# Optimization experiments

Measured on AMD Instinct MI355X. Metric: run time of the kernel, lower is better.

The kernel has to match this reference:

```python
import jax, jax.numpy as jnp
import numpy as np

C = 384          # input_channels
DH = 768         # dim_hidden
WS = 7           # window size (kernel_size)
NH = 12          # num_heads
HID = 3072       # mlp hidden = dim_hidden * mlp_ratio
NP = WS * WS     # 49 patch tokens
N = NP + 1       # + 1 cls token
SCALE = (C // NH) ** -0.5
REL_DIM = 2 * WS - 1


def _rel_pos_index():
    r = np.arange(WS)
    qx, qy = np.meshgrid(r, r, indexing='ij')
    q = np.stack([qx.ravel(), qy.ravel()], -1)                 # [NP,2], row-major flatten
    rel = q[:, None, :] - q[None, :, :] + WS - 1               # [NP,NP,2], values in [0,2ws-2]
    return jnp.asarray(rel[..., 0] * REL_DIM + rel[..., 1])    # [NP,NP]

REL_IDX = _rel_pos_index()


def layer_norm(x, g, b, eps=1e-5):
    m = jnp.mean(x, axis=-1, keepdims=True)
    v = jnp.var(x, axis=-1, keepdims=True)
    return (x - m) * jax.lax.rsqrt(v + eps) * g + b


def attention(x, w_qkv, w_proj, b_proj, rel_pos=None, mask=None):
    Bx, Nx, Cx = x.shape
    qkv = (x @ w_qkv.T).reshape(Bx, Nx, 3, NH, Cx // NH).transpose(2, 0, 3, 1, 4)
    q, k, v = qkv[0], qkv[1], qkv[2]                           # [B,H,N,d]
    attn = jnp.einsum('bhqd,bhkd->bhqk', q, k) * SCALE
    if rel_pos is not None:
        bias = rel_pos[REL_IDX].transpose(2, 0, 1)[None]       # [1,NH,NP,NP]
        attn = attn.at[:, :, 1:, 1:].add(bias)                 # skip cls token row/col
    if mask is not None:
        attn = attn + mask[:, None]                            # broadcast over heads
    attn = jax.nn.softmax(attn, axis=-1)
    y = jnp.einsum('bhqk,bhkd->bhqd', attn, v).transpose(0, 2, 1, 3).reshape(Bx, Nx, Cx)
    return y @ w_proj.T + b_proj


def setup_inputs() -> dict:
    key = jax.random.key(0)
    ks = jax.random.split(key, 16)
    s = 0.02
    BNW = 2048  # B * num_windows = 32 * 64
    return {
        'out': jax.random.normal(ks[0], (BNW, N, C), jnp.float32),
        'mask': jnp.zeros((BNW, N, N), jnp.float32),
        'g0': jnp.ones((C,), jnp.float32), 'b0': jnp.zeros((C,), jnp.float32),
        'g1': jnp.ones((C,), jnp.float32), 'b1': jnp.zeros((C,), jnp.float32),
        'g2': jnp.ones((C,), jnp.float32), 'b2': jnp.zeros((C,), jnp.float32),
        'ge': jnp.ones((C,), jnp.float32), 'be': jnp.zeros((C,), jnp.float32),
        'w_qkv': jax.random.normal(ks[1], (3 * C, C), jnp.float32) * s,
        'w_proj': jax.random.normal(ks[2], (C, C), jnp.float32) * s,
        'b_proj': jnp.zeros((C,), jnp.float32),
        'rel_pos': jax.random.normal(ks[3], (REL_DIM * REL_DIM, NH), jnp.float32) * s,
        'w_fc1': jax.random.normal(ks[4], (HID, C), jnp.float32) * s,
        'b_fc1': jnp.zeros((HID,), jnp.float32),
        'w_fc2': jax.random.normal(ks[5], (DH, HID), jnp.float32) * s,
        'b_fc2': jnp.zeros((DH,), jnp.float32),
        'w_exp': jax.random.normal(ks[6], (DH, C), jnp.float32) * s,
        'b_exp': jnp.zeros((DH,), jnp.float32),
        'w_lin': jax.random.normal(ks[7], (C, DH), jnp.float32) * s,
        'b_lin': jnp.zeros((C,), jnp.float32),
        'B': 32, 'H': 56, 'W': 56,
    }


def reference(out, mask, g0, b0, g1, b1, g2, b2, ge, be,
              w_qkv, w_proj, b_proj, rel_pos,
              w_fc1, b_fc1, w_fc2, b_fc2, w_exp, b_exp, w_lin, b_lin,
              B, H, W):
    Cc = out.shape[-1]
    # cls-token attention across windows of each image
    cls = out[:, :1].reshape(B, -1, Cc)                        # [B, nw, C]
    cls = cls + attention(layer_norm(cls, g0, b0), w_qkv, w_proj, b_proj)
    cls = cls.reshape(-1, 1, Cc)
    x = jnp.concatenate([cls, out[:, 1:]], axis=1)             # [B*nw, N, C]
    # windowed patch attention with rel-pos bias + mask
    x = x + attention(layer_norm(x, g1, b1), w_qkv, w_proj, b_proj,
                      rel_pos=rel_pos, mask=mask)
    # expand path: norm -> gelu -> linear (input_channels != dim_hidden)
    identity = jax.nn.gelu(layer_norm(x, ge, be), approximate=False) @ w_exp.T + b_exp
    # mlp path: norm -> fc1 -> gelu -> fc2
    h = layer_norm(x, g2, b2)
    h = jax.nn.gelu(h @ w_fc1.T + b_fc1, approximate=False)
    h = h @ w_fc2.T + b_fc2
    tmp = identity + h                                          # [B*nw, N, DH]
    return tmp @ w_lin.T + b_lin                                # [B*nw, N, C]
```

## Files before the change

kernel.cpp:

```cpp
#include <hip/hip_runtime.h>
#include <hip/hip_bf16.h>
#include <math.h>

#define NHEADS 12
#define NTOK   50
#define NWIN   2048
#define IMGS   32
#define CDIM   384
#define QKVD   1152
#define DHID   768
#define MLPH   3072
#define KTAIL  3456
#define SCALE_F 0.17677669529663687f

typedef short short8 __attribute__((ext_vector_type(8)));
typedef short short4v __attribute__((ext_vector_type(4)));
typedef short short2v __attribute__((ext_vector_type(2)));
typedef float f32x4  __attribute__((ext_vector_type(4)));
typedef __hip_bfloat16 bf16;

__device__ __forceinline__ float gelu_f(float x){
  return 0.5f*x*(1.0f+erff(x*0.7071067811865476f));
}
__device__ __forceinline__ short bfs(float x){
  bf16 h = __float2bfloat16(x); return *(short*)&h;
}

__global__ void cvt4_kernel(const float* s0, bf16* d0, int n0,
                            const float* s1, bf16* d1, int n1,
                            const float* s2, bf16* d2, int n2,
                            const float* s3, bf16* d3, int n3){
  int stride = gridDim.x*blockDim.x, g = blockIdx.x*blockDim.x + threadIdx.x;
  for (int i=g; i<n0; i+=stride) d0[i] = __float2bfloat16(s0[i]);
  for (int i=g; i<n1; i+=stride) d1[i] = __float2bfloat16(s1[i]);
  for (int i=g; i<n2; i+=stride) d2[i] = __float2bfloat16(s2[i]);
  for (int i=g; i<n3; i+=stride) d3[i] = __float2bfloat16(s3[i]);
}

__global__ __launch_bounds__(256) void transpose_cvt_kernel(const float* __restrict__ src,
    bf16* __restrict__ dst, int R, int Cc){
  __shared__ float tile[32][33];
  int bx = blockIdx.x, by = blockIdx.y;
  int c = threadIdx.x & 31, r0 = threadIdx.x >> 5;
  #pragma unroll
  for (int rr = r0; rr < 32; rr += 8)
    tile[rr][c] = src[(size_t)(by*32+rr)*Cc + bx*32 + c];
  __syncthreads();
  #pragma unroll
  for (int rr = r0; rr < 32; rr += 8)
    dst[(size_t)(bx*32+rr)*R + by*32 + c] = __float2bfloat16(tile[c][rr]);
}

__global__ void bias_combine_kernel(const float* __restrict__ wlin,
    const float* __restrict__ b_lin, const float* __restrict__ b_exp,
    const float* __restrict__ b_fc2, float* __restrict__ biasc){
  int i = blockIdx.x*blockDim.x + threadIdx.x;
  if (i >= CDIM) return;
  float s = b_lin[i];
  for (int d=0; d<DHID; d++) s += wlin[(size_t)i*DHID+d]*(b_exp[d]+b_fc2[d]);
  biasc[i] = s;
}

template<bool GELU>
__global__ __launch_bounds__(256) void ln_kernel(const float* __restrict__ x, long ldx,
    const float* __restrict__ g, const float* __restrict__ b,
    bf16* __restrict__ y, int rows)
{
  int row = blockIdx.x*4 + (threadIdx.x>>6);
  if (row >= rows) return;
  int l = threadIdx.x & 63;
  const float2* xr = (const float2*)(x + (size_t)row*ldx);
  float2 v[3]; float s = 0.f;
  #pragma unroll
  for (int j=0;j<3;j++){ v[j] = xr[l + 64*j]; s += v[j].x + v[j].y; }
  #pragma unroll
  for (int off=32; off; off>>=1) s += __shfl_xor(s, off, 64);
  float mean = s * (1.0f/384.0f);
  float vs = 0.f;
  #pragma unroll
  for (int j=0;j<3;j++){ float dx=v[j].x-mean, dy=v[j].y-mean; vs += dx*dx+dy*dy; }
  #pragma unroll
  for (int off=32; off; off>>=1) vs += __shfl_xor(vs, off, 64);
  float rstd = rsqrtf(vs*(1.0f/384.0f) + 1e-5f);
  short2v* yr = (short2v*)(y + (size_t)row*384);
  const float2* gv = (const float2*)g; const float2* bv = (const float2*)b;
  #pragma unroll
  for (int j=0;j<3;j++){
    float2 gg = gv[l+64*j], bb = bv[l+64*j];
    float o0 = (v[j].x-mean)*rstd*gg.x + bb.x;
    float o1 = (v[j].y-mean)*rstd*gg.y + bb.y;
    if (GELU){ o0 = gelu_f(o0); o1 = gelu_f(o1); }
    short2v pk; pk[0]=bfs(o0); pk[1]=bfs(o1);
    yr[l+64*j] = pk;
  }
}

__global__ __launch_bounds__(256) void ln_dual_kernel(const float* __restrict__ x,
    const float* __restrict__ ge, const float* __restrict__ be,
    const float* __restrict__ g2, const float* __restrict__ b2,
    bf16* __restrict__ yeo, long lde, bf16* __restrict__ y2o, int rows)
{
  int row = blockIdx.x*4 + (threadIdx.x>>6);
  if (row >= rows) return;
  int l = threadIdx.x & 63;
  const float2* xr = (const float2*)(x + (size_t)row*384);
  float2 v[3]; float s = 0.f;
  #pragma unroll
  for (int j=0;j<3;j++){ v[j] = xr[l + 64*j]; s += v[j].x + v[j].y; }
  #pragma unroll
  for (int off=32; off; off>>=1) s += __shfl_xor(s, off, 64);
  float mean = s * (1.0f/384.0f);
  float vs = 0.f;
  #pragma unroll
  for (int j=0;j<3;j++){ float dx=v[j].x-mean, dy=v[j].y-mean; vs += dx*dx+dy*dy; }
  #pragma unroll
  for (int off=32; off; off>>=1) vs += __shfl_xor(vs, off, 64);
  float rstd = rsqrtf(vs*(1.0f/384.0f) + 1e-5f);
  short2v* ye = (short2v*)(yeo + (size_t)row*lde);
  short2v* y2 = (short2v*)(y2o + (size_t)row*384);
  const float2* gev = (const float2*)ge; const float2* bev = (const float2*)be;
  const float2* g2v = (const float2*)g2; const float2* b2v = (const float2*)b2;
  #pragma unroll
  for (int j=0;j<3;j++){
    float n0 = (v[j].x-mean)*rstd, n1 = (v[j].y-mean)*rstd;
    float2 gg = gev[l+64*j], bb = bev[l+64*j];
    short2v pe; pe[0]=bfs(gelu_f(n0*gg.x+bb.x)); pe[1]=bfs(gelu_f(n1*gg.y+bb.y));
    ye[l+64*j] = pe;
    gg = g2v[l+64*j]; bb = b2v[l+64*j];
    short2v p2; p2[0]=bfs(n0*gg.x+bb.x); p2[1]=bfs(n1*gg.y+bb.y);
    y2[l+64*j] = p2;
  }
}

template<bool OUT_BF16, bool BIAS, int RES, bool GELU>
__device__ __forceinline__ void gemm_dev(
    const bf16* __restrict__ A, const bf16* __restrict__ B, void* Cv,
    const float* __restrict__ bias, const void* res,
    int M, int N, int K, int ldc, int ldres)
{
  __shared__ short As[3][128*32];
  __shared__ short Bs[3][128*32];
  const int t  = threadIdx.x;
  const int l  = t & 63;
  const int w  = t >> 6;
  const int wr = w >> 1, wc = w & 1;
  const int lr = l & 15, kg = l >> 4;

  const int nwg = gridDim.x * gridDim.y;
  const int lin = blockIdx.y * gridDim.x + blockIdx.x;
  const int q8 = nwg >> 3, r8 = nwg & 7;
  const int xcd = lin & 7, slot = lin >> 3;
  const int swz = (xcd < r8) ? (xcd*(q8+1) + slot) : (r8*(q8+1) + (xcd-r8)*q8 + slot);
  const int by = swz / gridDim.x, bx = swz - by*gridDim.x;

  const int bm = by * 128, bn = bx * 128;
  const short* Ag = (const short*)A;
  const short* Bg = (const short*)B;

  const int eo0 = w*1024 + l*8;
  const int rowS0 = eo0 >> 5, colS0 = eo0 & 31;
  const int eo1 = eo0 + 512;
  const int rowS1 = eo1 >> 5, colS1 = eo1 & 31;

  #define STAGE(k0, b) do { \
    __builtin_amdgcn_global_load_lds( \
      (const __attribute__((address_space(1))) void*)&Ag[(size_t)(bm+rowS0)*K + (k0) + colS0], \
      (__attribute__((address_space(3))) void*)((char*)&As[b][0] + w*2048), 16, 0, 0); \
    __builtin_amdgcn_global_load_lds( \
      (const __attribute__((address_space(1))) void*)&Bg[(size_t)(bn+rowS0)*K + (k0) + colS0], \
      (__attribute__((address_space(3))) void*)((char*)&Bs[b][0] + w*2048), 16, 0, 0); \
    __builtin_amdgcn_global_load_lds( \
      (const __attribute__((address_space(1))) void*)&Ag[(size_t)(bm+rowS1)*K + (k0) + colS1], \
      (__attribute__((address_space(3))) void*)((char*)&As[b][0] + w*2048 + 1024), 16, 0, 0); \
    __builtin_amdgcn_global_load_lds( \
      (const __attribute__((address_space(1))) void*)&Bg[(size_t)(bn+rowS1)*K + (k0) + colS1], \
      (__attribute__((address_space(3))) void*)((char*)&Bs[b][0] + w*2048 + 1024), 16, 0, 0); \
  } while(0)

  f32x4 acc[4][4] = {};

  STAGE(0, 0);
  STAGE(32, 1);
  asm volatile("s_waitcnt vmcnt(4)" ::: "memory");
  __builtin_amdgcn_s_barrier();

  int cur = 0, nb = 2;
  for (int k0 = 0; k0 < K; k0 += 32) {
    const bool more = (k0 + 64 < K);
    if (more) STAGE(k0 + 64, nb);

    short8 af[4], bfm[4];
    #pragma unroll
    for (int m=0;m<4;m++) af[m]  = *(const short8*)(&As[cur][(wr*64 + m*16 + lr)*32 + kg*8]);
    #pragma unroll
    for (int n=0;n<4;n++) bfm[n] = *(const short8*)(&Bs[cur][(wc*64 + n*16 + lr)*32 + kg*8]);
    __builtin_amdgcn_s_setprio(1);
    #pragma unroll
    for (int m=0;m<4;m++)
      #pragma unroll
      for (int n=0;n<4;n++)
        acc[m][n] = __builtin_amdgcn_mfma_f32_16x16x32_bf16(af[m], bfm[n], acc[m][n], 0,0,0);
    __builtin_amdgcn_s_setprio(0);

    if (more) { asm volatile("s_waitcnt vmcnt(4)" ::: "memory"); }
    else      { asm volatile("s_waitcnt vmcnt(0)" ::: "memory"); }
    __builtin_amdgcn_s_barrier();
    cur = (cur==2) ? 0 : cur+1;
    nb  = (nb==2)  ? 0 : nb+1;
  }
  #undef STAGE

  #pragma unroll
  for (int m=0;m<4;m++){
    int row0 = bm + wr*64 + m*16 + kg*4;
    #pragma unroll
    for (int n=0;n<4;n++){
      int col = bn + wc*64 + n*16 + lr;
      float bv = BIAS ? bias[col] : 0.0f;
      #pragma unroll
      for (int r=0;r<4;r++){
        float val = acc[m][n][r] + bv;
        if (RES == 1) val += ((const float*)res)[(size_t)(row0+r)*ldres + col];
        if (GELU) val = gelu_f(val);
        if (OUT_BF16) ((bf16*)Cv)[(size_t)(row0+r)*ldc + col] = __float2bfloat16(val);
        else          ((float*)Cv)[(size_t)(row0+r)*ldc + col] = val;
      }
    }
  }
}

#define GEMM_K(NAME, OB, BI, RE, GE) \
__global__ __launch_bounds__(256) void NAME( \
    const bf16* __restrict__ A, const bf16* __restrict__ B, void* Cv, \
    const float* __restrict__ bias, const void* res, \
    int M, int N, int K, int ldc, int ldres){ \
  gemm_dev<OB,BI,RE,GE>(A,B,Cv,bias,res,M,N,K,ldc,ldres); }

GEMM_K(gemm_qkv_k,  true,  false, 0, false)
GEMM_K(gemm_proj_k, false, true,  1, false)
GEMM_K(gemm_fc1_k,  true,  true,  0, true)
GEMM_K(gemm_tail_k, false, true,  0, false)
GEMM_K(gemm_wcmb_k, true,  false, 0, false)

__global__ __launch_bounds__(256) void attn_cls_kernel(const bf16* __restrict__ qkv,
                                                       bf16* __restrict__ y)
{
  int img = blockIdx.x, h = blockIdx.y;
  __shared__ float q[64][33], k[64][33], v[64][33];
  __shared__ float s[64][65];
  int t = threadIdx.x;
  for (int idx=t; idx<64*32; idx+=256){
    int i = idx>>5, d = idx&31;
    const bf16* base = qkv + ((size_t)(img*64+i))*QKVD + h*32 + d;
    q[i][d] = __bfloat162float(base[0]);
    k[i][d] = __bfloat162float(base[384]);
    v[i][d] = __bfloat162float(base[768]);
  }
  __syncthreads();
  for (int idx=t; idx<64*64; idx+=256){
    int i = idx>>6, j = idx&63;
    float a = 0.f;
    #pragma unroll
    for (int d=0; d<32; d++) a += q[i][d]*k[j][d];
    s[i][j] = a * SCALE_F;
  }
  __syncthreads();
  if (t < 64){
    float m = -1e30f;
    for (int j=0;j<64;j++) m = fmaxf(m, s[t][j]);
    float sum = 0.f;
    for (int j=0;j<64;j++){ float e = __expf(s[t][j]-m); s[t][j]=e; sum+=e; }
    float inv = 1.0f/sum;
    for (int j=0;j<64;j++) s[t][j] *= inv;
  }
  __syncthreads();
  for (int idx=t; idx<64*32; idx+=256){
    int i = idx>>5, d = idx&31;
    float a = 0.f;
    for (int j=0;j<64;j++) a += s[i][j]*v[j][d];
    y[((size_t)(img*64+i))*CDIM + h*32 + d] = __float2bfloat16(a);
  }
}

__global__ __launch_bounds__(64) void attn_win_mfma(const bf16* __restrict__ qkv,
    const float* __restrict__ mask, const float* __restrict__ rel_pos,
    bf16* __restrict__ y)
{
  const int lw = blockIdx.x, h = blockIdx.y;
  const int l = threadIdx.x;
  const int lr = l & 15, kg = l >> 4;
  __shared__ short Plds[64*72];
  __shared__ short VTl[32*72];
  __shared__ float rp[169];

  const size_t tok0 = (size_t)lw * NTOK;
  const short* qbase = (const short*)qkv;

  for (int i=l; i<169; i+=64) rp[i] = rel_pos[i*NHEADS + h];

  short8 qf[4], kf[4];
  #pragma unroll
  for (int n=0;n<4;n++){
    int qt = 16*n + lr;
    if (qt < 50) qf[n] = *(const short8*)&qbase[(tok0+qt)*QKVD + h*32 + kg*8];
    else         qf[n] = short8(0);
  }
  #pragma unroll
  for (int m=0;m<4;m++){
    int kt = 16*m + lr;
    if (kt < 50) kf[m] = *(const short8*)&qbase[(tok0+kt)*QKVD + 384 + h*32 + kg*8];
    else         kf[m] = short8(0);
  }

  {
    short vv[32];
    if (l < 50){
      const short8* vp = (const short8*)&qbase[(tok0+l)*QKVD + 768 + h*32];
      #pragma unroll
      for (int jj=0;jj<4;jj++){ short8 xv = vp[jj];
        #pragma unroll
        for (int e=0;e<8;e++) vv[jj*8+e] = xv[e]; }
    } else {
      #pragma unroll
      for (int d=0; d<32; d++) vv[d]=0;
    }
    #pragma unroll
    for (int d=0; d<32; d++) VTl[d*72 + l] = vv[d];
  }

  f32x4 sacc[4][4] = {};
  #pragma unroll
  for (int m=0;m<4;m++)
    #pragma unroll
    for (int n=0;n<4;n++)
      sacc[m][n] = __builtin_amdgcn_mfma_f32_16x16x32_bf16(kf[m], qf[n], sacc[m][n], 0,0,0);

  const float* mrow = mask + (size_t)lw*2500;
  float sv[4][4][4];
  #pragma unroll
  for (int m=0;m<4;m++){
    #pragma unroll
    for (int r=0;r<4;r++){
      int kt = 16*m + 4*kg + r;
      #pragma unroll
      for (int n=0;n<4;n++){
        int qt = 16*n + lr;
        float a;
        if (kt < 50 && qt < 50){
          a = sacc[m][n][r] * SCALE_F;
          if (kt>=1 && qt>=1){
            int qi=qt-1, kj=kt-1;
            int ridx = ((qi/7)-(kj/7)+6)*13 + (qi%7)-(kj%7)+6;
            a += rp[ridx];
          }
          a += mrow[qt*50+kt];
        } else a = -1e30f;
        sv[m][r][n] = a;
      }
    }
  }

  #pragma unroll
  for (int n=0;n<4;n++){
    float mx = -1e30f;
    #pragma unroll
    for (int m=0;m<4;m++)
      #pragma unroll
      for (int r=0;r<4;r++) mx = fmaxf(mx, sv[m][r][n]);
    mx = fmaxf(mx, __shfl_xor(mx, 16));
    mx = fmaxf(mx, __shfl_xor(mx, 32));
    float sum = 0.f;
    float pv[4][4];
    #pragma unroll
    for (int m=0;m<4;m++)
      #pragma unroll
      for (int r=0;r<4;r++){ float p = __expf(sv[m][r][n]-mx); pv[m][r]=p; sum+=p; }
    sum += __shfl_xor(sum, 16);
    sum += __shfl_xor(sum, 32);
    float inv = 1.0f/sum;
    int qrow = (16*n + lr)*72;
    #pragma unroll
    for (int m=0;m<4;m++){
      short4v pk;
      #pragma unroll
      for (int r=0;r<4;r++) pk[r] = bfs(pv[m][r]*inv);
      *(short4v*)&Plds[qrow + 16*m + 4*kg] = pk;
    }
  }
  __syncthreads();

  f32x4 oacc[2][4] = {};
  #pragma unroll
  for (int ks=0; ks<2; ks++){
    short8 pf[4];
    #pragma unroll
    for (int n=0;n<4;n++)
      pf[n] = *(const short8*)&Plds[(16*n+lr)*72 + 32*ks + kg*8];
    #pragma unroll
    for (int md=0; md<2; md++){
      short8 vf = *(const short8*)&VTl[(16*md+lr)*72 + 32*ks + kg*8];
      #pragma unroll
      for (int n=0;n<4;n++)
        oacc[md][n] = __builtin_amdgcn_mfma_f32_16x16x32_bf16(vf, pf[n], oacc[md][n], 0,0,0);
    }
  }

  short* yb = (short*)y;
  #pragma unroll
  for (int n=0;n<4;n++){
    int qt = 16*n + lr;
    if (qt >= 50) continue;
    #pragma unroll
    for (int md=0; md<2; md++){
      short4v pk;
      #pragma unroll
      for (int r=0;r<4;r++) pk[r] = bfs(oacc[md][n][r]);
      *(short4v*)&yb[(tok0+qt)*CDIM + h*32 + 16*md + 4*kg] = pk;
    }
  }
}

extern "C" void kernel_launch(void* const* d_in, const int* in_sizes, int n_in,
                              void* d_out, int out_size, void* d_ws, size_t ws_size,
                              hipStream_t stream)
{
  const float* x_in   = (const float*)d_in[0];
  const float* maskp  = (const float*)d_in[1];
  const float* g0 = (const float*)d_in[2];  const float* b0 = (const float*)d_in[3];
  const float* g1 = (const float*)d_in[4];  const float* b1 = (const float*)d_in[5];
  const float* g2 = (const float*)d_in[6];  const float* b2 = (const float*)d_in[7];
  const float* ge = (const float*)d_in[8];  const float* be = (const float*)d_in[9];
  const float* w_qkv = (const float*)d_in[10];
  const float* w_proj= (const float*)d_in[11];
  const float* b_proj= (const float*)d_in[12];
  const float* rel_pos=(const float*)d_in[13];
  const float* w_fc1 = (const float*)d_in[14];
  const float* b_fc1 = (const float*)d_in[15];
  const float* w_fc2 = (const float*)d_in[16];
  const float* b_fc2 = (const float*)d_in[17];
  const float* w_exp = (const float*)d_in[18];
  const float* b_exp = (const float*)d_in[19];
  const float* w_lin = (const float*)d_in[20];
  const float* b_lin = (const float*)d_in[21];
  float* dout = (float*)d_out;

  const size_t NT = (size_t)NWIN * NTOK;

  size_t off = 0;
  auto alloc = [&](size_t bytes)->void* {
    void* p = (char*)d_ws + off;
    off += (bytes + 255) & ~(size_t)255;
    return p;
  };

  bf16* wqkv_b = (bf16*)alloc((size_t)QKVD*CDIM*2);
  bf16* wproj_b= (bf16*)alloc((size_t)CDIM*CDIM*2);
  bf16* wfc1_b = (bf16*)alloc((size_t)MLPH*CDIM*2);
  bf16* wlin_b = (bf16*)alloc((size_t)CDIM*DHID*2);
  bf16* wexpT_b= (bf16*)alloc((size_t)CDIM*DHID*2);
  bf16* wfc2T_b= (bf16*)alloc((size_t)MLPH*DHID*2);
  bf16* W_comb = (bf16*)alloc((size_t)CDIM*KTAIL*2);
  float* biasc = (float*)alloc((size_t)CDIM*4);
  float* xb    = (float*)alloc(NT*CDIM*4);
  bf16* clsln  = (bf16*)alloc((size_t)NWIN*CDIM*2);
  bf16* qkvcls = (bf16*)alloc((size_t)NWIN*QKVD*2);
  bf16* ycls   = (bf16*)alloc((size_t)NWIN*CDIM*2);

  int CH_W = 2048;
  const size_t per_window = 537600ull;
  while (CH_W > 128 && off + (size_t)CH_W*per_window + 16384 > ws_size) CH_W >>= 1;
  const int CH_T = CH_W * NTOK;

  bf16*  xln   = (bf16*) alloc((size_t)CH_T*CDIM*2);
  bf16*  qkvc  = (bf16*) alloc((size_t)CH_T*QKVD*2);
  bf16*  ybfc  = (bf16*) alloc((size_t)CH_T*CDIM*2);
  bf16*  h1ext = (bf16*) alloc((size_t)CH_T*KTAIL*2);

  cvt4_kernel<<<512, 256, 0, stream>>>(
      w_qkv, wqkv_b, QKVD*CDIM,  w_proj, wproj_b, CDIM*CDIM,
      w_fc1, wfc1_b, MLPH*CDIM,  w_lin,  wlin_b,  CDIM*DHID);
  transpose_cvt_kernel<<<dim3(CDIM/32, DHID/32), 256, 0, stream>>>(w_exp, wexpT_b, DHID, CDIM);
  transpose_cvt_kernel<<<dim3(MLPH/32, DHID/32), 256, 0, stream>>>(w_fc2, wfc2T_b, DHID, MLPH);
  bias_combine_kernel<<<6, 64, 0, stream>>>(w_lin, b_lin, b_exp, b_fc2, biasc);
  gemm_wcmb_k<<<dim3(CDIM/128, CDIM/128), 256, 0, stream>>>(
      wlin_b, wexpT_b, W_comb, nullptr, nullptr, CDIM, CDIM, DHID, KTAIL, 0);
  gemm_wcmb_k<<<dim3(MLPH/128, CDIM/128), 256, 0, stream>>>(
      wlin_b, wfc2T_b, W_comb + 384, nullptr, nullptr, CDIM, MLPH, DHID, KTAIL, 0);

  hipMemcpyAsync(xb, x_in, NT*CDIM*4, hipMemcpyDeviceToDevice, stream);

  ln_kernel<false><<<NWIN/4, 256, 0, stream>>>(x_in, (long)NTOK*CDIM, g0, b0, clsln, NWIN);
  gemm_qkv_k<<<dim3(QKVD/128, NWIN/128), 256, 0, stream>>>(
      clsln, wqkv_b, qkvcls, nullptr, nullptr, NWIN, QKVD, CDIM, QKVD, 0);
  attn_cls_kernel<<<dim3(IMGS, NHEADS), 256, 0, stream>>>(qkvcls, ycls);
  gemm_proj_k<<<dim3(CDIM/128, NWIN/128), 256, 0, stream>>>(
      ycls, wproj_b, xb, b_proj, x_in, NWIN, CDIM, CDIM, NTOK*CDIM, NTOK*CDIM);

  const int nch = NWIN / CH_W;
  for (int c = 0; c < nch; c++){
    int w0 = c * CH_W;
    size_t t0 = (size_t)w0 * NTOK;
    float* xbc = xb + t0*CDIM;
    float* doutc = dout + t0*CDIM;
    int MT = CH_T, MB = CH_T/128;

    ln_kernel<false><<<MT/4, 256, 0, stream>>>(xbc, CDIM, g1, b1, xln, MT);
    gemm_qkv_k<<<dim3(QKVD/128, MB), 256, 0, stream>>>(
        xln, wqkv_b, qkvc, nullptr, nullptr, MT, QKVD, CDIM, QKVD, 0);
    attn_win_mfma<<<dim3(CH_W, NHEADS), 64, 0, stream>>>(
        qkvc, maskp + (size_t)w0*2500, rel_pos, ybfc);
    gemm_proj_k<<<dim3(CDIM/128, MB), 256, 0, stream>>>(
        ybfc, wproj_b, xbc, b_proj, xbc, MT, CDIM, CDIM, CDIM, CDIM);

    ln_dual_kernel<<<MT/4, 256, 0, stream>>>(xbc, ge, be, g2, b2, h1ext, KTAIL, ybfc, MT);

    gemm_fc1_k<<<dim3(MLPH/128, MB), 256, 0, stream>>>(
        ybfc, wfc1_b, h1ext + 384, b_fc1, nullptr, MT, MLPH, CDIM, KTAIL, 0);

    gemm_tail_k<<<dim3(CDIM/128, MB), 256, 0, stream>>>(
        h1ext, W_comb, doutc, biasc, nullptr, MT, CDIM, KTAIL, CDIM, 0);
  }
}
```

Baseline: 1.826 ms.

## Fuse fc1+GELU with folded fc2/lin GEMM, keeping hidden activations on-chip

Replaces the fc1 GEMM that wrote a 3072-wide bf16 hidden buffer, and the separate tail GEMM that re-read it, with one fused kernel. Each 64-row block computes fc1+GELU in 128-column chunks into LDS and accumulates immediately into the pre-folded W_lin·W_fc2 product. The expand path becomes a separate small GEMM that writes the output first, and the fused kernel adds onto it. This removes large HBM round trips for the hidden activations and shrinks workspace. In exchange it reads the weights from global memory per block without LDS staging, and uses 64-row blocks with heavy register use, which may limit occupancy.

Measured after the change: 2.210 ms. 1.21x slower.

```diff
diff --git a/kernel.cpp b/kernel.cpp
--- a/kernel.cpp
+++ b/kernel.cpp
@@ -10,7 +10,6 @@
 #define QKVD   1152
 #define DHID   768
 #define MLPH   3072
-#define KTAIL  3456
 #define SCALE_F 0.17677669529663687f
 
 typedef short short8 __attribute__((ext_vector_type(8)));
@@ -98,7 +97,7 @@
 __global__ __launch_bounds__(256) void ln_dual_kernel(const float* __restrict__ x,
     const float* __restrict__ ge, const float* __restrict__ be,
     const float* __restrict__ g2, const float* __restrict__ b2,
-    bf16* __restrict__ yeo, long lde, bf16* __restrict__ y2o, int rows)
+    bf16* __restrict__ yeo, bf16* __restrict__ y2o, int rows)
 {
   int row = blockIdx.x*4 + (threadIdx.x>>6);
   if (row >= rows) return;
@@ -116,7 +115,7 @@
   #pragma unroll
   for (int off=32; off; off>>=1) vs += __shfl_xor(vs, off, 64);
   float rstd = rsqrtf(vs*(1.0f/384.0f) + 1e-5f);
-  short2v* ye = (short2v*)(yeo + (size_t)row*lde);
+  short2v* ye = (short2v*)(yeo + (size_t)row*384);
   short2v* y2 = (short2v*)(y2o + (size_t)row*384);
   const float2* gev = (const float2*)ge; const float2* bev = (const float2*)be;
   const float2* g2v = (const float2*)g2; const float2* b2v = (const float2*)b2;
@@ -238,9 +237,95 @@
 
 GEMM_K(gemm_qkv_k,  true,  false, 0, false)
 GEMM_K(gemm_proj_k, false, true,  1, false)
-GEMM_K(gemm_fc1_k,  true,  true,  0, true)
-GEMM_K(gemm_tail_k, false, true,  0, false)
+GEMM_K(gemm_cex_k,  false, true,  0, false)
 GEMM_K(gemm_wcmb_k, true,  false, 0, false)
+
+__global__ __launch_bounds__(256, 2) void fused_tail_k(
+    const bf16* __restrict__ xln2,
+    const bf16* __restrict__ wfc1,
+    const float* __restrict__ bfc1,
+    const bf16* __restrict__ wh,
+    float* __restrict__ dout)
+{
+  constexpr int RP = 392;
+  constexpr int HP = 136;
+  __shared__ short A2[64*RP];
+  __shared__ short Hh[64*HP];
+  const int l = threadIdx.x & 63, w = threadIdx.x >> 6;
+  const int lr = l & 15, kg = l >> 4;
+  const int bm = blockIdx.x * 64;
+  const short* X  = (const short*)xln2;
+  const short* WF = (const short*)wfc1;
+  const short* WC = (const short*)wh;
+
+  f32x4 acc[6][4];
+  #pragma unroll
+  for (int i=0;i<6;i++)
+    #pragma unroll
+    for (int j=0;j<4;j++)
+      acc[i][j] = *(const f32x4*)&dout[(size_t)(bm+16*j+lr)*384 + w*96 + 16*i + 4*kg];
+
+  #pragma unroll
+  for (int i=0;i<12;i++){
+    int c = threadIdx.x + 256*i;
+    int row = c / 48, slot = c - row*48;
+    *(short8*)&A2[row*RP + slot*8] = *(const short8*)&X[(size_t)(bm+row)*384 + slot*8];
+  }
+  __syncthreads();
+
+  for (int nc = 0; nc < 24; nc++){
+    const int fc0 = nc*128 + w*32;
+    f32x4 c1[4][2] = {};
+    #pragma unroll
+    for (int ks=0; ks<12; ks++){
+      short8 a[4], b[2];
+      #pragma unroll
+      for (int m=0;m<4;m++) a[m] = *(const short8*)&A2[(16*m+lr)*RP + ks*32 + kg*8];
+      #pragma unroll
+      for (int n=0;n<2;n++)
+        b[n] = *(const short8*)&WF[(size_t)(fc0 + 16*n + lr)*384 + ks*32 + kg*8];
+      #pragma unroll
+      for (int m=0;m<4;m++)
+        #pragma unroll
+        for (int n=0;n<2;n++)
+          c1[m][n] = __builtin_amdgcn_mfma_f32_16x16x32_bf16(a[m], b[n], c1[m][n], 0,0,0);
+    }
+    float bb0 = bfc1[fc0 + lr], bb1 = bfc1[fc0 + 16 + lr];
+    __syncthreads();
+    #pragma unroll
+    for (int m=0;m<4;m++)
+      #pragma unroll
+      for (int r=0;r<4;r++){
+        int hrow = (16*m + 4*kg + r)*HP + w*32;
+        Hh[hrow + lr]      = bfs(gelu_f(c1[m][0][r] + bb0));
+        Hh[hrow + 16 + lr] = bfs(gelu_f(c1[m][1][r] + bb1));
+      }
+    __syncthreads();
+
+    #pragma unroll
+    for (int ks=0; ks<4; ks++){
+      short8 hb[4], wa[6];
+      #pragma unroll
+      for (int j=0;j<4;j++) hb[j] = *(const short8*)&Hh[(16*j+lr)*HP + ks*32 + kg*8];
+      #pragma unroll
+      for (int i=0;i<6;i++)
+        wa[i] = *(const short8*)&WC[(size_t)(w*96 + 16*i + lr)*3072 + nc*128 + ks*32 + kg*8];
+      __builtin_amdgcn_s_setprio(1);
+      #pragma unroll
+      for (int i=0;i<6;i++)
+        #pragma unroll
+        for (int j=0;j<4;j++)
+          acc[i][j] = __builtin_amdgcn_mfma_f32_16x16x32_bf16(wa[i], hb[j], acc[i][j], 0,0,0);
+      __builtin_amdgcn_s_setprio(0);
+    }
+  }
+
+  #pragma unroll
+  for (int i=0;i<6;i++)
+    #pragma unroll
+    for (int j=0;j<4;j++)
+      *(f32x4*)&dout[(size_t)(bm+16*j+lr)*384 + w*96 + 16*i + 4*kg] = acc[i][j];
+}
 
 __global__ __launch_bounds__(256) void attn_cls_kernel(const bf16* __restrict__ qkv,
                                                        bf16* __restrict__ y)
@@ -459,7 +544,8 @@
   bf16* wlin_b = (bf16*)alloc((size_t)CDIM*DHID*2);
   bf16* wexpT_b= (bf16*)alloc((size_t)CDIM*DHID*2);
   bf16* wfc2T_b= (bf16*)alloc((size_t)MLPH*DHID*2);
-  bf16* W_comb = (bf16*)alloc((size_t)CDIM*KTAIL*2);
+  bf16* W_el   = (bf16*)alloc((size_t)CDIM*CDIM*2);
+  bf16* W_h    = (bf16*)alloc((size_t)CDIM*MLPH*2);
   float* biasc = (float*)alloc((size_t)CDIM*4);
   float* xb    = (float*)alloc(NT*CDIM*4);
   bf16* clsln  = (bf16*)alloc((size_t)NWIN*CDIM*2);
@@ -467,14 +553,14 @@
   bf16* ycls   = (bf16*)alloc((size_t)NWIN*CDIM*2);
 
   int CH_W = 2048;
-  const size_t per_window = 537600ull;
+  const size_t per_window = 230400ull;
   while (CH_W > 128 && off + (size_t)CH_W*per_window + 16384 > ws_size) CH_W >>= 1;
   const int CH_T = CH_W * NTOK;
 
   bf16*  xln   = (bf16*) alloc((size_t)CH_T*CDIM*2);
   bf16*  qkvc  = (bf16*) alloc((size_t)CH_T*QKVD*2);
   bf16*  ybfc  = (bf16*) alloc((size_t)CH_T*CDIM*2);
-  bf16*  h1ext = (bf16*) alloc((size_t)CH_T*KTAIL*2);
+  bf16*  xlnE  = (bf16*) alloc((size_t)CH_T*CDIM*2);
 
   cvt4_kernel<<<512, 256, 0, stream>>>(
       w_qkv, wqkv_b, QKVD*CDIM,  w_proj, wproj_b, CDIM*CDIM,
@@ -483,9 +569,9 @@
   transpose_cvt_kernel<<<dim3(MLPH/32, DHID/32), 256, 0, stream>>>(w_fc2, wfc2T_b, DHID, MLPH);
   bias_combine_kernel<<<6, 64, 0, stream>>>(w_lin, b_lin, b_exp, b_fc2, biasc);
   gemm_wcmb_k<<<dim3(CDIM/128, CDIM/128), 256, 0, stream>>>(
-      wlin_b, wexpT_b, W_comb, nullptr, nullptr, CDIM, CDIM, DHID, KTAIL, 0);
+      wlin_b, wexpT_b, W_el, nullptr, nullptr, CDIM, CDIM, DHID, CDIM, 0);
   gemm_wcmb_k<<<dim3(MLPH/128, CDIM/128), 256, 0, stream>>>(
-      wlin_b, wfc2T_b, W_comb + 384, nullptr, nullptr, CDIM, MLPH, DHID, KTAIL, 0);
+      wlin_b, wfc2T_b, W_h, nullptr, nullptr, CDIM, MLPH, DHID, MLPH, 0);
 
   hipMemcpyAsync(xb, x_in, NT*CDIM*4, hipMemcpyDeviceToDevice, stream);
 
@@ -512,12 +598,12 @@
     gemm_proj_k<<<dim3(CDIM/128, MB), 256, 0, stream>>>(
         ybfc, wproj_b, xbc, b_proj, xbc, MT, CDIM, CDIM, CDIM, CDIM);
 
-    ln_dual_kernel<<<MT/4, 256, 0, stream>>>(xbc, ge, be, g2, b2, h1ext, KTAIL, ybfc, MT);
-
-    gemm_fc1_k<<<dim3(MLPH/128, MB), 256, 0, stream>>>(
-        ybfc, wfc1_b, h1ext + 384, b_fc1, nullptr, MT, MLPH, CDIM, KTAIL, 0);
-
-    gemm_tail_k<<<dim3(CDIM/128, MB), 256, 0, stream>>>(
-        h1ext, W_comb, doutc, biasc, nullptr, MT, CDIM, KTAIL, CDIM, 0);
-  }
-}
+    ln_dual_kernel<<<MT/4, 256, 0, stream>>>(xbc, ge, be, g2, b2, xlnE, ybfc, MT);
+
+    gemm_cex_k<<<dim3(CDIM/128, MB), 256, 0, stream>>>(
+        xlnE, W_el, doutc, biasc, nullptr, MT, CDIM, CDIM, CDIM, 0);
+
+    fused_tail_k<<<MT/64, 256, 0, stream>>>(
+        ybfc, wfc1_b, b_fc1, W_h, doutc);
+  }
+}
```
